# Performance work log

Hardware: AMD Instinct MI355X
Metric: run time of the kernel (lower is better)

The kernel has to match this reference:

```python
import jax, jax.numpy as jnp
import numpy as np

B, N, D, E = 2, 2048, 768, 8
H = 4 * D
TARGET_SPARSITY = 0.6
K_KEEP = int(N * (1.0 - TARGET_SPARSITY))  # positions kept per sequence
V_MAX, FEAT_CLAMP, ETA = 3.0, 10.0, 1.0


def setup_inputs() -> dict:
    key = jax.random.key(0)
    ks = jax.random.split(key, 8)
    s = 0.02
    return {
        "x": jax.random.normal(ks[0], (B, N, D), jnp.float32),
        "Wg": jax.random.normal(ks[1], (D, E), jnp.float32) * s,
        "bg": jnp.zeros((E,), jnp.float32),
        "W1": jax.random.normal(ks[2], (E, D, H), jnp.float32) * s,
        "b1": jnp.zeros((E, H), jnp.float32),
        "W2": jax.random.normal(ks[3], (E, H, D), jnp.float32) * s,
        "b2": jnp.zeros((E, D), jnp.float32),
        "Wv": jax.random.normal(ks[4], (D,), jnp.float32) * s,
        "bv": jnp.zeros((), jnp.float32),
        "Wm": jax.random.normal(ks[5], (D,), jnp.float32) * s,
        "bm": jnp.zeros((), jnp.float32),
        "Wo": jax.random.normal(ks[6], (2, D), jnp.float32) * s,
        "bo": jnp.zeros((D,), jnp.float32),
        "bk_scale": jnp.ones((), jnp.float32),
    }


def _bk_gii(v):
    """Diagonal of (T - i*eta*I)^{-1}, T tridiagonal with diag v, off-diag 1.
    Continued-fraction recursions: a_i = d_i - 1/a_{i-1} (fwd), b_i = d_i - 1/b_{i+1} (bwd),
    G_ii = 1/(a_i + b_i - d_i). Complex arithmetic done in explicit (re, im) pairs."""
    dr, di = v, jnp.full_like(v, -ETA)  # (B, N)

    def cf(reverse):
        init = (jnp.full((v.shape[0],), 1e18, v.dtype), jnp.zeros((v.shape[0],), v.dtype))
        def step(c, d):
            ar, ai = c
            drr, dii = d
            den = ar * ar + ai * ai  # 1/a_prev ~ 0 at init (1e18^2 < f32 max)
            out = (drr - ar / den, dii + ai / den)
            return out, out
        _, (r, i) = jax.lax.scan(step, init, (dr.T, di.T), reverse=reverse)
        return r.T, i.T  # (B, N)

    ar, ai = cf(False)
    br, bi = cf(True)
    cr, ci = ar + br - dr, ai + bi - di
    den = cr * cr + ci * ci
    return cr / den, -ci / den


def reference(x, Wg, bg, W1, b1, W2, b2, Wv, bv, Wm, bm, Wo, bo, bk_scale):
    # --- top-1 MoE FFN (eval mode: dropout off) ---
    probs = jax.nn.softmax(x @ Wg + bg, axis=-1)                     # (B,N,E)
    top_p = jnp.max(probs, axis=-1)                                  # top-1 gate weight
    comb = jax.nn.one_hot(jnp.argmax(probs, -1), E, dtype=x.dtype) * top_p[..., None]
    h = jax.nn.gelu(jnp.einsum('bnd,edh->ebnh', x, W1) + b1[:, None, None, :])
    y = jnp.einsum('ebnh,ehd->ebnd', h, W2) + b2[:, None, None, :]
    ffn_out = jnp.einsum('ebnd,bne->bnd', y, comb)                   # (B,N,D)

    # --- per-token potential v ---
    v = jnp.clip(ffn_out @ Wv + bv, -V_MAX, V_MAX)                   # (B,N)

    # --- learned sparsity mask: keep top-K gate scores per sequence ---
    scores = jax.nn.sigmoid(x @ Wm + bm)                             # (B,N)
    thr = jax.lax.top_k(scores, K_KEEP)[0][:, -1]
    mask = (scores >= thr[:, None]).astype(x.dtype)

    # --- sparse BK-Core diagonal resolvent features (Re, Im) ---
    gr, gi = _bk_gii(v)
    feats = jnp.clip(jnp.stack([gr, gi], -1) * mask[..., None], -FEAT_CLAMP, FEAT_CLAMP)

    return ffn_out + bk_scale * (feats @ Wo + bo)                    # (B,N,D)
```

## Files before the change

### kernel.cpp

```cpp
#include <hip/hip_runtime.h>

typedef unsigned short ushort_t;
typedef unsigned int uint32;

#define NTOK 4096
#define SEQ 2048
#define DDIM 768
#define HDIM 3072
#define NEXP 8
#define KKEEP 819
#define MTILE 128
#define MAXTILES 40
#define MAXSLOTS 5120

typedef __attribute__((ext_vector_type(8))) short bfrag8;
typedef __attribute__((ext_vector_type(4))) float facc4;

__device__ __forceinline__ ushort_t f2bf(float f) {
  uint32 x = __float_as_uint(f);
  uint32 r = (x + 0x7FFFu + ((x >> 16) & 1u)) >> 16;
  return (ushort_t)r;
}
__device__ __forceinline__ float gelu_f(float u) {
  float z = u + 0.044715f * u * u * u;
  float e = __builtin_amdgcn_exp2f(-2.3021840216f * z);
  return u * __builtin_amdgcn_rcpf(1.f + e);
}

#define GL2LDS(gp, lp)                                                        \
  __builtin_amdgcn_global_load_lds(                                           \
      (const __attribute__((address_space(1))) void*)(gp),                    \
      (__attribute__((address_space(3))) void*)(lp), 16, 0, 0)

__global__ __launch_bounds__(256) void k_gate(
    const float* __restrict__ x, const float* __restrict__ Wg,
    const float* __restrict__ bg, const float* __restrict__ Wm,
    const float* __restrict__ bm, const float* __restrict__ bv,
    int* __restrict__ expert, float* __restrict__ topp,
    float* __restrict__ score, float* __restrict__ v) {
  int tid = threadIdx.x, lane = tid & 63, w = tid >> 6;
  int t = blockIdx.x * 4 + w;
  float g[8];
#pragma unroll
  for (int e = 0; e < 8; ++e) g[e] = 0.f;
  float sm = 0.f;
  for (int d = lane; d < DDIM; d += 64) {
    float xv = x[(size_t)t * DDIM + d];
    float4 w0 = *(const float4*)(Wg + d * 8);
    float4 w1 = *(const float4*)(Wg + d * 8 + 4);
    g[0] += xv * w0.x; g[1] += xv * w0.y; g[2] += xv * w0.z; g[3] += xv * w0.w;
    g[4] += xv * w1.x; g[5] += xv * w1.y; g[6] += xv * w1.z; g[7] += xv * w1.w;
    sm += xv * Wm[d];
  }
#pragma unroll
  for (int e = 0; e < 8; ++e) {
#pragma unroll
    for (int off = 32; off > 0; off >>= 1) g[e] += __shfl_down(g[e], off, 64);
  }
#pragma unroll
  for (int off = 32; off > 0; off >>= 1) sm += __shfl_down(sm, off, 64);
  if (lane == 0) {
    float l[8];
#pragma unroll
    for (int e = 0; e < 8; ++e) l[e] = g[e] + bg[e];
    int am = 0;
    float mx = l[0];
#pragma unroll
    for (int e = 1; e < 8; ++e) {
      if (l[e] > mx) { mx = l[e]; am = e; }
    }
    float s = 0.f;
#pragma unroll
    for (int e = 0; e < 8; ++e) s += expf(l[e] - mx);
    expert[t] = am;
    topp[t] = 1.f / s;
    float z = sm + bm[0];
    score[t] = 1.f / (1.f + expf(-z));
    v[t] = bv[0];
  }
}

__global__ __launch_bounds__(256) void k_thrbucket(
    const float* __restrict__ score, float* __restrict__ thr,
    const int* __restrict__ expert, int* __restrict__ meta,
    int* __restrict__ tiles, int* __restrict__ slot_token) {
  int tid = threadIdx.x;
  if (blockIdx.x < 2) {
    int b = blockIdx.x;
    __shared__ uint32 chist[256];
    __shared__ float vals[2048];
    __shared__ uint32 scnt;
    __shared__ int bstar_s, kprime_s;
    chist[tid] = 0;
    if (tid == 0) scnt = 0;
    __syncthreads();
    for (int i = tid; i < SEQ; i += 256) {
      float s = score[b * SEQ + i];
      int bin = min(255, max(0, (int)(s * 256.f)));
      atomicAdd(&chist[bin], 1u);
    }
    __syncthreads();
    if (tid == 0) {
      int cum = 0;
      for (int j = 255; j >= 0; --j) {
        cum += (int)chist[j];
        if (cum >= KKEEP) {
          bstar_s = j;
          kprime_s = KKEEP - (cum - (int)chist[j]);
          break;
        }
      }
    }
    __syncthreads();
    int bstar = bstar_s, kprime = kprime_s;
    for (int i = tid; i < SEQ; i += 256) {
      float s = score[b * SEQ + i];
      int bin = min(255, max(0, (int)(s * 256.f)));
      if (bin == bstar) vals[atomicAdd(&scnt, 1u)] = s;
    }
    __syncthreads();
    int n = (int)scnt;
    for (int ci = tid; ci < n; ci += 256) {
      float xx = vals[ci];
      int g = 0, eq = 0;
      for (int j = 0; j < n; ++j) {
        g += (vals[j] > xx);
        eq += (vals[j] == xx);
      }
      if (g < kprime && kprime <= g + eq) thr[b] = xx;
    }
  } else {
    __shared__ int cnt[NEXP];
    __shared__ int off[NEXP];
    if (tid < NEXP) cnt[tid] = 0;
    __syncthreads();
    for (int t = tid; t < NTOK; t += 256) atomicAdd(&cnt[expert[t]], 1);
    __syncthreads();
    if (tid == 0) {
      int run = 0, nt = 0;
      for (int e = 0; e < NEXP; ++e) {
        off[e] = run;
        int c = cnt[e];
        int padded = (c + MTILE - 1) / MTILE * MTILE;
        for (int s = 0; s < padded; s += MTILE)
          tiles[nt++] = (e << 16) | (run + s);
        run += padded;
      }
      meta[0] = nt;
      meta[1] = run;
    }
    __syncthreads();
    for (int s = tid; s < MAXSLOTS; s += 256) slot_token[s] = -1;
    __syncthreads();
    for (int t = tid; t < NTOK; t += 256) {
      int p = atomicAdd(&off[expert[t]], 1);
      slot_token[p] = t;
    }
  }
}

__device__ __forceinline__ void wtile_transpose(const float* __restrict__ src,
                                                ushort_t* __restrict__ dst,
                                                int K, int N, int nkb, int bi,
                                                int tid, float (*t)[65]) {
  int per_e = nkb * (N / 64);
  int e = bi / per_e, rem = bi % per_e;
  int k0 = (rem % nkb) * 64, n0 = (rem / nkb) * 64;
  const float* S = src + (size_t)e * K * N;
  ushort_t* D = dst + (size_t)e * N * K;
  int r = tid >> 4, c4 = (tid & 15) * 4;
#pragma unroll
  for (int it = 0; it < 4; ++it) {
    int k = r + it * 16;
    float4 vv = *(const float4*)(S + (size_t)(k0 + k) * N + n0 + c4);
    t[k][c4] = vv.x; t[k][c4 + 1] = vv.y; t[k][c4 + 2] = vv.z; t[k][c4 + 3] = vv.w;
  }
  __syncthreads();
#pragma unroll
  for (int it = 0; it < 4; ++it) {
    int n = r + it * 16;
    ushort4 o;
    o.x = f2bf(t[c4][n]); o.y = f2bf(t[c4 + 1][n]);
    o.z = f2bf(t[c4 + 2][n]); o.w = f2bf(t[c4 + 3][n]);
    *(ushort4*)(D + (size_t)(n0 + n) * K + k0 + c4) = o;
  }
}

__global__ __launch_bounds__(256) void k_prep(
    const float* __restrict__ x, const int* __restrict__ slot_token,
    ushort_t* __restrict__ xp, const float* __restrict__ W1,
    ushort_t* __restrict__ W1t, const float* __restrict__ W2,
    ushort_t* __restrict__ W2t) {
  __shared__ float t[64][65];
  int bx = blockIdx.x;
  int tid = threadIdx.x;
  if (bx < MAXSLOTS) {
    int tok = slot_token[bx];
    for (int d = tid; d < DDIM; d += 256) {
      float vv = (tok >= 0) ? x[(size_t)tok * DDIM + d] : 0.f;
      xp[(size_t)bx * DDIM + d] = f2bf(vv);
    }
    return;
  }
  if (bx < MAXSLOTS + 4608) {
    wtile_transpose(W1, W1t, 768, 3072, 12, bx - MAXSLOTS, tid, t);
  } else {
    wtile_transpose(W2, W2t, 3072, 768, 48, bx - MAXSLOTS - 4608, tid, t);
  }
}

__global__ __launch_bounds__(256) void k_wt(const float* __restrict__ src,
                                            ushort_t* __restrict__ dst, int K,
                                            int N, int nkb) {
  __shared__ float t[64][65];
  wtile_transpose(src, dst, K, N, nkb, blockIdx.x, threadIdx.x, t);
}

__global__ __launch_bounds__(256) void k_gemm1(
    const ushort_t* __restrict__ xp, const ushort_t* __restrict__ Wt,
    const float* __restrict__ b1, const int* __restrict__ meta,
    const int* __restrict__ tiles, ushort_t* __restrict__ h) {
  __shared__ ushort_t As[128 * 64];
  __shared__ ushort_t Bs[128 * 64];
  if ((int)blockIdx.x >= meta[0]) return;
  int desc = tiles[blockIdx.x];
  int e = desc >> 16, slot0 = desc & 0xFFFF;
  int n0 = blockIdx.y * 128;
  int tid = threadIdx.x;
  int lane = tid & 63, w = tid >> 6;
  int mq = (w & 1) << 6, nq = (w >> 1) << 6;
  int mrow = lane & 15, quad = lane >> 4;
  int rl = tid >> 3;
  int sw = (tid & 7) ^ (rl & 7);
  const ushort_t* Ag = xp + (size_t)(slot0 + rl) * 768 + sw * 8;
  const ushort_t* Bg = Wt + ((size_t)e * 3072 + n0 + rl) * 768 + sw * 8;
  facc4 acc[4][4];
  facc4 zero = {0.f, 0.f, 0.f, 0.f};
#pragma unroll
  for (int i = 0; i < 4; ++i)
#pragma unroll
    for (int j = 0; j < 4; ++j) acc[i][j] = zero;
  for (int k0 = 0; k0 < 768; k0 += 64) {
#pragma unroll
    for (int r = 0; r < 4; ++r) {
      GL2LDS(Ag + k0 + (size_t)r * 32 * 768, As + (r * 256 + tid) * 8);
      GL2LDS(Bg + k0 + (size_t)r * 32 * 768, Bs + (r * 256 + tid) * 8);
    }
    __syncthreads();
#pragma unroll
    for (int kk = 0; kk < 2; ++kk) {
      bfrag8 a[4], b[4];
      int ph = (((kk << 2) + quad) ^ (mrow & 7)) << 3;
#pragma unroll
      for (int i = 0; i < 4; ++i)
        a[i] = *(const bfrag8*)(As + ((mq + i * 16 + mrow) << 6) + ph);
#pragma unroll
      for (int j = 0; j < 4; ++j)
        b[j] = *(const bfrag8*)(Bs + ((nq + j * 16 + mrow) << 6) + ph);
#pragma unroll
      for (int i = 0; i < 4; ++i)
#pragma unroll
        for (int j = 0; j < 4; ++j)
          acc[i][j] = __builtin_amdgcn_mfma_f32_16x16x32_bf16(a[i], b[j],
                                                              acc[i][j], 0, 0, 0);
    }
    __syncthreads();
  }
  const float* bb = b1 + (size_t)e * 3072 + n0;
#pragma unroll
  for (int i = 0; i < 4; ++i) {
    int mo = mq + i * 16 + (quad << 2);
#pragma unroll
    for (int j = 0; j < 4; ++j) {
      int nc = nq + j * 16 + mrow;
      float bias = bb[nc];
#pragma unroll
      for (int r = 0; r < 4; ++r) {
        float val = gelu_f(acc[i][j][r] + bias);
        h[(size_t)(slot0 + mo + r) * 3072 + n0 + nc] = f2bf(val);
      }
    }
  }
}

__global__ __launch_bounds__(256) void k_gemm2(
    const ushort_t* __restrict__ h, const ushort_t* __restrict__ Wt,
    const float* __restrict__ b2, const float* __restrict__ topp,
    const float* __restrict__ Wv, const int* __restrict__ meta,
    const int* __restrict__ tiles, const int* __restrict__ slot_token,
    float* __restrict__ outf, float* __restrict__ v) {
  __shared__ ushort_t As[64 * 64];
  __shared__ ushort_t Bs[64 * 64];
  if ((int)blockIdx.x >= meta[0]) return;
  int desc = tiles[blockIdx.x];
  int e = desc >> 16;
  int slot0 = (desc & 0xFFFF) + ((int)blockIdx.z << 6);
  int n0 = blockIdx.y * 64;
  int tid = threadIdx.x;
  int lane = tid & 63, w = tid >> 6;
  int mq = (w & 1) << 5;
  int nq = (w >> 1) << 5;
  int mrow = lane & 15, quad = lane >> 4;
  int rl = tid >> 3;
  int sw = (tid & 7) ^ (rl & 7);
  const ushort_t* Ag = h + (size_t)(slot0 + rl) * 3072 + sw * 8;
  const ushort_t* Bg = Wt + ((size_t)e * 768 + n0 + rl) * 3072 + sw * 8;
  facc4 acc[2][2];
  facc4 zero = {0.f, 0.f, 0.f, 0.f};
#pragma unroll
  for (int i = 0; i < 2; ++i)
#pragma unroll
    for (int j = 0; j < 2; ++j) acc[i][j] = zero;
  for (int k0 = 0; k0 < 3072; k0 += 64) {
#pragma unroll
    for (int r = 0; r < 2; ++r) {
      GL2LDS(Ag + k0 + (size_t)r * 32 * 3072, As + (r * 256 + tid) * 8);
      GL2LDS(Bg + k0 + (size_t)r * 32 * 3072, Bs + (r * 256 + tid) * 8);
    }
    __syncthreads();
#pragma unroll
    for (int kk = 0; kk < 2; ++kk) {
      bfrag8 a[2], b[2];
      int ph = (((kk << 2) + quad) ^ (mrow & 7)) << 3;
#pragma unroll
      for (int i = 0; i < 2; ++i)
        a[i] = *(const bfrag8*)(As + ((mq + i * 16 + mrow) << 6) + ph);
#pragma unroll
      for (int j = 0; j < 2; ++j)
        b[j] = *(const bfrag8*)(Bs + ((nq + j * 16 + mrow) << 6) + ph);
#pragma unroll
      for (int i = 0; i < 2; ++i)
#pragma unroll
        for (int j = 0; j < 2; ++j)
          acc[i][j] = __builtin_amdgcn_mfma_f32_16x16x32_bf16(a[i], b[j],
                                                              acc[i][j], 0, 0, 0);
    }
    __syncthreads();
  }
  const float* bb = b2 + (size_t)e * 768 + n0;
  float wv0 = Wv[n0 + nq + mrow];
  float wv1 = Wv[n0 + nq + 16 + mrow];
  float bb0 = bb[nq + mrow], bb1 = bb[nq + 16 + mrow];
#pragma unroll
  for (int i = 0; i < 2; ++i) {
    int mo = mq + i * 16 + (quad << 2);
#pragma unroll
    for (int r = 0; r < 4; ++r) {
      int slot = slot0 + mo + r;
      int tok = slot_token[slot];
      if (tok < 0) continue;
      float tp = topp[tok];
      float f0 = tp * (acc[i][0][r] + bb0);
      float f1 = tp * (acc[i][1][r] + bb1);
      outf[(size_t)tok * 768 + n0 + nq + mrow] = f0;
      outf[(size_t)tok * 768 + n0 + nq + 16 + mrow] = f1;
      float pv = f0 * wv0 + f1 * wv1;
#pragma unroll
      for (int off = 8; off > 0; off >>= 1) pv += __shfl_down(pv, off, 16);
      if (mrow == 0) atomicAdd(&v[tok], pv);
    }
  }
}

struct CM {
  float ar, ai, br, bi, cr, ci, dr, di;
};
__device__ __forceinline__ CM cmmul(const CM& A, const CM& B) {
  CM C;
  C.ar = A.ar * B.ar - A.ai * B.ai + A.br * B.cr - A.bi * B.ci;
  C.ai = A.ar * B.ai + A.ai * B.ar + A.br * B.ci + A.bi * B.cr;
  C.br = A.ar * B.br - A.ai * B.bi + A.br * B.dr - A.bi * B.di;
  C.bi = A.ar * B.bi + A.ai * B.br + A.br * B.di + A.bi * B.dr;
  C.cr = A.cr * B.ar - A.ci * B.ai + A.dr * B.cr - A.di * B.ci;
  C.ci = A.cr * B.ai + A.ci * B.ar + A.dr * B.ci + A.di * B.cr;
  C.dr = A.cr * B.br - A.ci * B.bi + A.dr * B.dr - A.di * B.di;
  C.di = A.cr * B.bi + A.ci * B.br + A.dr * B.di + A.di * B.dr;
  return C;
}
__device__ __forceinline__ void cmnorm(CM& A) {
  float m = fmaxf(fmaxf(fmaxf(fabsf(A.ar), fabsf(A.ai)),
                        fmaxf(fabsf(A.br), fabsf(A.bi))),
                  fmaxf(fmaxf(fabsf(A.cr), fabsf(A.ci)),
                        fmaxf(fabsf(A.dr), fabsf(A.di))));
  float s = 1.0f / fmaxf(m, 1e-30f);
  A.ar *= s; A.ai *= s; A.br *= s; A.bi *= s;
  A.cr *= s; A.ci *= s; A.dr *= s; A.di *= s;
}
__device__ __forceinline__ CM cmshfl_up(const CM& A, int off) {
  CM B;
  B.ar = __shfl_up(A.ar, off, 64); B.ai = __shfl_up(A.ai, off, 64);
  B.br = __shfl_up(A.br, off, 64); B.bi = __shfl_up(A.bi, off, 64);
  B.cr = __shfl_up(A.cr, off, 64); B.ci = __shfl_up(A.ci, off, 64);
  B.dr = __shfl_up(A.dr, off, 64); B.di = __shfl_up(A.di, off, 64);
  return B;
}

__global__ __launch_bounds__(256) void k_bkscan(
    const float* __restrict__ v, float* __restrict__ Ar, float* __restrict__ Ai,
    float* __restrict__ Br, float* __restrict__ Bi) {
  int b = blockIdx.x >> 1, rev = blockIdx.x & 1;
  int tid = threadIdx.x, lane = tid & 63, wv = tid >> 6;
  const float* vb = v + b * SEQ;
  float dv[8];
  int sbase = tid * 8;
#pragma unroll
  for (int q = 0; q < 8; ++q) {
    int s = sbase + q;
    int n = rev ? (SEQ - 1 - s) : s;
    dv[q] = fminf(3.f, fmaxf(-3.f, vb[n]));
  }
  CM L;
  L.ar = dv[0]; L.ai = -1.f; L.br = -1.f; L.bi = 0.f;
  L.cr = 1.f; L.ci = 0.f; L.dr = 0.f; L.di = 0.f;
#pragma unroll
  for (int q = 1; q < 8; ++q) {
    float dr = dv[q];
    float nar = dr * L.ar + L.ai - L.cr;
    float nai = dr * L.ai - L.ar - L.ci;
    float nbr = dr * L.br + L.bi - L.dr;
    float nbi = dr * L.bi - L.br - L.di;
    L.cr = L.ar; L.ci = L.ai; L.dr = L.br; L.di = L.bi;
    L.ar = nar; L.ai = nai; L.br = nbr; L.bi = nbi;
  }
  cmnorm(L);
  CM I = L;
#pragma unroll
  for (int off = 1; off < 64; off <<= 1) {
    CM P = cmshfl_up(I, off);
    if (lane >= off) {
      I = cmmul(I, P);
      cmnorm(I);
    }
  }
  __shared__ float wag[4][8];
  if (lane == 63) {
    wag[wv][0] = I.ar; wag[wv][1] = I.ai; wag[wv][2] = I.br; wag[wv][3] = I.bi;
    wag[wv][4] = I.cr; wag[wv][5] = I.ci; wag[wv][6] = I.dr; wag[wv][7] = I.di;
  }
  __syncthreads();
  CM E = cmshfl_up(I, 1);
  if (lane == 0) {
    E.ar = 1.f; E.ai = 0.f; E.br = 0.f; E.bi = 0.f;
    E.cr = 0.f; E.ci = 0.f; E.dr = 1.f; E.di = 0.f;
  }
  for (int j = wv - 1; j >= 0; --j) {
    CM Aj;
    Aj.ar = wag[j][0]; Aj.ai = wag[j][1]; Aj.br = wag[j][2]; Aj.bi = wag[j][3];
    Aj.cr = wag[j][4]; Aj.ci = wag[j][5]; Aj.dr = wag[j][6]; Aj.di = wag[j][7];
    E = cmmul(E, Aj);
    cmnorm(E);
  }
  float u0r = E.ar, u0i = E.ai, u1r = E.cr, u1i = E.ci;
  float* Rr = rev ? Br : Ar;
  float* Ri = rev ? Bi : Ai;
#pragma unroll
  for (int q = 0; q < 8; ++q) {
    float dr = dv[q];
    float n0r = dr * u0r + u0i - u1r;
    float n0i = dr * u0i - u0r - u1i;
    u1r = u0r; u1i = u0i; u0r = n0r; u0i = n0i;
    float m = fmaxf(fmaxf(fabsf(u0r), fabsf(u0i)), fmaxf(fabsf(u1r), fabsf(u1i)));
    float sc = 1.f / fmaxf(m, 1e-30f);
    u0r *= sc; u0i *= sc; u1r *= sc; u1i *= sc;
    float den = u1r * u1r + u1i * u1i;
    float arr = (u0r * u1r + u0i * u1i) / den;
    float aii = (u0i * u1r - u0r * u1i) / den;
    int s = sbase + q;
    int n = rev ? (SEQ - 1 - s) : s;
    Rr[b * SEQ + n] = arr;
    Ri[b * SEQ + n] = aii;
  }
}

__global__ __launch_bounds__(256) void k_final(
    float* __restrict__ outf, const float* __restrict__ v,
    const float* __restrict__ Ar, const float* __restrict__ Ai,
    const float* __restrict__ Br, const float* __restrict__ Bi,
    const float* __restrict__ score, const float* __restrict__ thr,
    const float* __restrict__ Wo, const float* __restrict__ bo,
    const float* __restrict__ bk) {
  int t = blockIdx.x;
  int b = t >> 11;
  float vc = fminf(3.f, fmaxf(-3.f, v[t]));
  float cr = Ar[t] + Br[t] - vc;
  float ci = Ai[t] + Bi[t] + 1.f;
  float den = cr * cr + ci * ci;
  float gr = cr / den, gi = -ci / den;
  bool m = (score[t] >= thr[b]);
  float fr = m ? fminf(10.f, fmaxf(-10.f, gr)) : 0.f;
  float fi = m ? fminf(10.f, fmaxf(-10.f, gi)) : 0.f;
  float bs = bk[0];
  for (int d = threadIdx.x; d < DDIM; d += 256) {
    float o = outf[(size_t)t * DDIM + d] +
              bs * (fr * Wo[d] + fi * Wo[DDIM + d] + bo[d]);
    outf[(size_t)t * DDIM + d] = o;
  }
}

extern "C" void kernel_launch(void* const* d_in, const int* in_sizes, int n_in,
                              void* d_out, int out_size, void* d_ws, size_t ws_size,
                              hipStream_t stream) {
  const float* x  = (const float*)d_in[0];
  const float* Wg = (const float*)d_in[1];
  const float* bg = (const float*)d_in[2];
  const float* W1 = (const float*)d_in[3];
  const float* b1 = (const float*)d_in[4];
  const float* W2 = (const float*)d_in[5];
  const float* b2 = (const float*)d_in[6];
  const float* Wv = (const float*)d_in[7];
  const float* bv = (const float*)d_in[8];
  const float* Wm = (const float*)d_in[9];
  const float* bm = (const float*)d_in[10];
  const float* Wo = (const float*)d_in[11];
  const float* bo = (const float*)d_in[12];
  const float* bk = (const float*)d_in[13];
  float* outf = (float*)d_out;

  unsigned char* w = (unsigned char*)d_ws;
  int*   expert     = (int*)(w + 0);
  float* topp       = (float*)(w + 16384);
  float* score      = (float*)(w + 32768);
  float* v          = (float*)(w + 49152);
  float* Ar         = (float*)(w + 65536);
  float* Ai         = (float*)(w + 81920);
  float* Br         = (float*)(w + 98304);
  float* Bi         = (float*)(w + 114688);
  float* thr        = (float*)(w + 131072);
  int*   meta       = (int*)(w + 131104);
  int*   tiles      = (int*)(w + 131136);
  int*   slot_token = (int*)(w + 131328);
  ushort_t* xp      = (ushort_t*)(w + 152064);
  ushort_t* h       = (ushort_t*)(w + 8016384);
  ushort_t* W1t     = (ushort_t*)(w + 39473664);
  size_t w2t_off = 39473664ull + 37748736ull;
  size_t need    = w2t_off + 37748736ull;
  bool fused = (ws_size >= need);
  ushort_t* W2t = fused ? (ushort_t*)(w + w2t_off) : W1t;

  k_gate<<<1024, 256, 0, stream>>>(x, Wg, bg, Wm, bm, bv, expert, topp, score, v);
  k_thrbucket<<<3, 256, 0, stream>>>(score, thr, expert, meta, tiles, slot_token);

  if (fused) {
    k_prep<<<MAXSLOTS + 9216, 256, 0, stream>>>(x, slot_token, xp, W1, W1t, W2,
                                                W2t);
    k_gemm1<<<dim3(MAXTILES, 24), 256, 0, stream>>>(xp, W1t, b1, meta, tiles, h);
    k_gemm2<<<dim3(MAXTILES, 12, 2), 256, 0, stream>>>(h, W2t, b2, topp, Wv,
                                                       meta, tiles, slot_token,
                                                       outf, v);
  } else {
    k_prep<<<MAXSLOTS + 4608, 256, 0, stream>>>(x, slot_token, xp, W1, W1t, W2,
                                                W2t);
    k_gemm1<<<dim3(MAXTILES, 24), 256, 0, stream>>>(xp, W1t, b1, meta, tiles, h);
    k_wt<<<4608, 256, 0, stream>>>(W2, W1t, 3072, 768, 48);
    k_gemm2<<<dim3(MAXTILES, 12, 2), 256, 0, stream>>>(h, W1t, b2, topp, Wv,
                                                       meta, tiles, slot_token,
                                                       outf, v);
  }

  k_bkscan<<<4, 256, 0, stream>>>(v, Ar, Ai, Br, Bi);
  k_final<<<NTOK, 256, 0, stream>>>(outf, v, Ar, Ai, Br, Bi, score, thr, Wo, bo, bk);
}
```

Baseline: 335.1 us.

## Overlap weight transposes with gate and GEMM1 kernels via extra blocks

Moves the W1 fp32-to-bf16 transpose into extra blocks of the gate kernel and the W2 transpose into extra blocks of the GEMM1 kernel, leaving k_prep to only gather tokens. The aim is to hide the weight-conversion bandwidth behind otherwise underutilized kernels (the gate kernel and the partially idle GEMM1 grid) instead of running it serially in k_prep. GEMM1 now uses a flattened 1D grid and a shared smem buffer reused as the transpose scratch. The gate kernel also gains a 16.6KB shared array, which may lower its occupancy.

```diff
diff --git a/kernel.cpp b/kernel.cpp
--- a/kernel.cpp
+++ b/kernel.cpp
@@ -12,6 +12,7 @@
 #define MTILE 128
 #define MAXTILES 40
 #define MAXSLOTS 5120
+#define NB1 (MAXTILES * 24)
 
 typedef __attribute__((ext_vector_type(8))) short bfrag8;
 typedef __attribute__((ext_vector_type(4))) float facc4;
@@ -31,14 +32,48 @@
   __builtin_amdgcn_global_load_lds(                                           \
       (const __attribute__((address_space(1))) void*)(gp),                    \
       (__attribute__((address_space(3))) void*)(lp), 16, 0, 0)
+
+__device__ __forceinline__ void wtile_transpose(const float* __restrict__ src,
+                                                ushort_t* __restrict__ dst,
+                                                int K, int N, int nkb, int bi,
+                                                int tid, float (*t)[65]) {
+  int per_e = nkb * (N / 64);
+  int e = bi / per_e, rem = bi % per_e;
+  int k0 = (rem % nkb) * 64, n0 = (rem / nkb) * 64;
+  const float* S = src + (size_t)e * K * N;
+  ushort_t* D = dst + (size_t)e * N * K;
+  int r = tid >> 4, c4 = (tid & 15) * 4;
+#pragma unroll
+  for (int it = 0; it < 4; ++it) {
+    int k = r + it * 16;
+    float4 vv = *(const float4*)(S + (size_t)(k0 + k) * N + n0 + c4);
+    t[k][c4] = vv.x; t[k][c4 + 1] = vv.y; t[k][c4 + 2] = vv.z; t[k][c4 + 3] = vv.w;
+  }
+  __syncthreads();
+#pragma unroll
+  for (int it = 0; it < 4; ++it) {
+    int n = r + it * 16;
+    ushort4 o;
+    o.x = f2bf(t[c4][n]); o.y = f2bf(t[c4 + 1][n]);
+    o.z = f2bf(t[c4 + 2][n]); o.w = f2bf(t[c4 + 3][n]);
+    *(ushort4*)(D + (size_t)(n0 + n) * K + k0 + c4) = o;
+  }
+}
 
 __global__ __launch_bounds__(256) void k_gate(
     const float* __restrict__ x, const float* __restrict__ Wg,
     const float* __restrict__ bg, const float* __restrict__ Wm,
     const float* __restrict__ bm, const float* __restrict__ bv,
     int* __restrict__ expert, float* __restrict__ topp,
-    float* __restrict__ score, float* __restrict__ v) {
-  int tid = threadIdx.x, lane = tid & 63, w = tid >> 6;
+    float* __restrict__ score, float* __restrict__ v,
+    const float* __restrict__ W1, ushort_t* __restrict__ W1t) {
+  __shared__ float ts[64][65];
+  int tid = threadIdx.x;
+  if ((int)blockIdx.x >= 1024) {
+    wtile_transpose(W1, W1t, 768, 3072, 12, (int)blockIdx.x - 1024, tid, ts);
+    return;
+  }
+  int lane = tid & 63, w = tid >> 6;
   int t = blockIdx.x * 4 + w;
   float g[8];
 #pragma unroll
@@ -159,53 +194,15 @@
   }
 }
 
-__device__ __forceinline__ void wtile_transpose(const float* __restrict__ src,
-                                                ushort_t* __restrict__ dst,
-                                                int K, int N, int nkb, int bi,
-                                                int tid, float (*t)[65]) {
-  int per_e = nkb * (N / 64);
-  int e = bi / per_e, rem = bi % per_e;
-  int k0 = (rem % nkb) * 64, n0 = (rem / nkb) * 64;
-  const float* S = src + (size_t)e * K * N;
-  ushort_t* D = dst + (size_t)e * N * K;
-  int r = tid >> 4, c4 = (tid & 15) * 4;
-#pragma unroll
-  for (int it = 0; it < 4; ++it) {
-    int k = r + it * 16;
-    float4 vv = *(const float4*)(S + (size_t)(k0 + k) * N + n0 + c4);
-    t[k][c4] = vv.x; t[k][c4 + 1] = vv.y; t[k][c4 + 2] = vv.z; t[k][c4 + 3] = vv.w;
-  }
-  __syncthreads();
-#pragma unroll
-  for (int it = 0; it < 4; ++it) {
-    int n = r + it * 16;
-    ushort4 o;
-    o.x = f2bf(t[c4][n]); o.y = f2bf(t[c4 + 1][n]);
-    o.z = f2bf(t[c4 + 2][n]); o.w = f2bf(t[c4 + 3][n]);
-    *(ushort4*)(D + (size_t)(n0 + n) * K + k0 + c4) = o;
-  }
-}
-
 __global__ __launch_bounds__(256) void k_prep(
     const float* __restrict__ x, const int* __restrict__ slot_token,
-    ushort_t* __restrict__ xp, const float* __restrict__ W1,
-    ushort_t* __restrict__ W1t, const float* __restrict__ W2,
-    ushort_t* __restrict__ W2t) {
-  __shared__ float t[64][65];
+    ushort_t* __restrict__ xp) {
   int bx = blockIdx.x;
   int tid = threadIdx.x;
-  if (bx < MAXSLOTS) {
-    int tok = slot_token[bx];
-    for (int d = tid; d < DDIM; d += 256) {
-      float vv = (tok >= 0) ? x[(size_t)tok * DDIM + d] : 0.f;
-      xp[(size_t)bx * DDIM + d] = f2bf(vv);
-    }
-    return;
-  }
-  if (bx < MAXSLOTS + 4608) {
-    wtile_transpose(W1, W1t, 768, 3072, 12, bx - MAXSLOTS, tid, t);
-  } else {
-    wtile_transpose(W2, W2t, 3072, 768, 48, bx - MAXSLOTS - 4608, tid, t);
+  int tok = slot_token[bx];
+  for (int d = tid; d < DDIM; d += 256) {
+    float vv = (tok >= 0) ? x[(size_t)tok * DDIM + d] : 0.f;
+    xp[(size_t)bx * DDIM + d] = f2bf(vv);
   }
 }
 
@@ -219,14 +216,23 @@
 __global__ __launch_bounds__(256) void k_gemm1(
     const ushort_t* __restrict__ xp, const ushort_t* __restrict__ Wt,
     const float* __restrict__ b1, const int* __restrict__ meta,
-    const int* __restrict__ tiles, ushort_t* __restrict__ h) {
-  __shared__ ushort_t As[128 * 64];
-  __shared__ ushort_t Bs[128 * 64];
-  if ((int)blockIdx.x >= meta[0]) return;
-  int desc = tiles[blockIdx.x];
+    const int* __restrict__ tiles, ushort_t* __restrict__ h,
+    const float* __restrict__ W2, ushort_t* __restrict__ W2t) {
+  __shared__ ushort_t smem[16384];
+  int tid = threadIdx.x;
+  int bid = blockIdx.x;
+  if (bid >= NB1) {
+    wtile_transpose(W2, W2t, 3072, 768, 48, bid - NB1,
+                    tid, reinterpret_cast<float(*)[65]>(smem));
+    return;
+  }
+  ushort_t* As = smem;
+  ushort_t* Bs = smem + 8192;
+  int tile = bid % MAXTILES, ny = bid / MAXTILES;
+  if (tile >= meta[0]) return;
+  int desc = tiles[tile];
   int e = desc >> 16, slot0 = desc & 0xFFFF;
-  int n0 = blockIdx.y * 128;
-  int tid = threadIdx.x;
+  int n0 = ny * 128;
   int lane = tid & 63, w = tid >> 6;
   int mq = (w & 1) << 6, nq = (w >> 1) << 6;
   int mrow = lane & 15, quad = lane >> 4;
@@ -537,20 +543,19 @@
   bool fused = (ws_size >= need);
   ushort_t* W2t = fused ? (ushort_t*)(w + w2t_off) : W1t;
 
-  k_gate<<<1024, 256, 0, stream>>>(x, Wg, bg, Wm, bm, bv, expert, topp, score, v);
+  k_gate<<<1024 + 4608, 256, 0, stream>>>(x, Wg, bg, Wm, bm, bv, expert, topp,
+                                          score, v, W1, W1t);
   k_thrbucket<<<3, 256, 0, stream>>>(score, thr, expert, meta, tiles, slot_token);
+  k_prep<<<MAXSLOTS, 256, 0, stream>>>(x, slot_token, xp);
 
   if (fused) {
-    k_prep<<<MAXSLOTS + 9216, 256, 0, stream>>>(x, slot_token, xp, W1, W1t, W2,
-                                                W2t);
-    k_gemm1<<<dim3(MAXTILES, 24), 256, 0, stream>>>(xp, W1t, b1, meta, tiles, h);
+    k_gemm1<<<NB1 + 4608, 256, 0, stream>>>(xp, W1t, b1, meta, tiles, h, W2,
+                                            W2t);
     k_gemm2<<<dim3(MAXTILES, 12, 2), 256, 0, stream>>>(h, W2t, b2, topp, Wv,
                                                        meta, tiles, slot_token,
                                                        outf, v);
   } else {
-    k_prep<<<MAXSLOTS + 4608, 256, 0, stream>>>(x, slot_token, xp, W1, W1t, W2,
-                                                W2t);
-    k_gemm1<<<dim3(MAXTILES, 24), 256, 0, stream>>>(xp, W1t, b1, meta, tiles, h);
+    k_gemm1<<<NB1, 256, 0, stream>>>(xp, W1t, b1, meta, tiles, h, W2, W2t);
     k_wt<<<4608, 256, 0, stream>>>(W2, W1t, 3072, 768, 48);
     k_gemm2<<<dim3(MAXTILES, 12, 2), 256, 0, stream>>>(h, W1t, b2, topp, Wv,
                                                        meta, tiles, slot_token,
```

Measured after the change: 326.4 us. -2.6%, faster.
